# Performance work log

Measured on AMD Instinct MI355X. Metric: run time of the kernel, lower is better.

## Reference

```python
import jax, jax.numpy as jnp
import numpy as np

N, D, K, NUM_PAIRS = 8192, 128, 128, 262144


def setup_inputs() -> dict:
    rng = np.random.default_rng(0)
    labels = rng.integers(0, K, size=N).astype(np.int32)
    # positive pairs: off-diagonal (i,j) with labels[i]==labels[j], same as
    # (diag_mask * match).nonzero() in torch; take a fixed deterministic prefix.
    match = labels[:, None] == labels[None, :]
    np.fill_diagonal(match, False)
    pi, pj = np.nonzero(match)
    assert pi.shape[0] >= NUM_PAIRS
    pos_idx = np.stack([pi[:NUM_PAIRS], pj[:NUM_PAIRS]], axis=1).astype(np.int32)
    # negative pairs: vectorized rejection sampling of (i,j) with labels differing
    neg_chunks, need = [], NUM_PAIRS
    while need > 0:
        cand = rng.integers(0, N, size=(2 * need, 2))
        ok = labels[cand[:, 0]] != labels[cand[:, 1]]
        cand = cand[ok][:need]
        neg_chunks.append(cand)
        need -= cand.shape[0]
    neg_idx = np.concatenate(neg_chunks, axis=0).astype(np.int32)
    key = jax.random.key(0)
    k1, k2 = jax.random.split(key)
    return {
        "Xemb": jax.random.normal(k1, (N, D), dtype=jnp.float32),
        "scores": jax.random.normal(k2, (N,), dtype=jnp.float32),  # unused by forward, kept for signature fidelity
        "h_bias": jnp.asarray(1.0, dtype=jnp.float32),
        "labels": jnp.asarray(labels),
        "pos_idx": jnp.asarray(pos_idx),
        "neg_idx": jnp.asarray(neg_idx),
    }


def reference(Xemb, scores, h_bias, labels, pos_idx, neg_idx):
    bias = jax.nn.softplus(h_bias)
    # positive pairs: squared euclidean distance
    dpos = Xemb[pos_idx[:, 0]] - Xemb[pos_idx[:, 1]]          # [P, D]
    pos_distances_sq = jnp.sum(dpos * dpos, axis=1)           # [P]
    # negative pairs: euclidean distance with margin (softplus bias)
    dneg = Xemb[neg_idx[:, 0]] - Xemb[neg_idx[:, 1]]          # [P, D]
    neg_distances = jnp.sqrt(jnp.sum(dneg * dneg, axis=1))    # [P]
    pos_loss = 0.5 * jnp.mean(pos_distances_sq)
    neg_loss = 0.5 * jnp.mean(jax.nn.relu(bias - neg_distances) ** 2)
    return jnp.stack([pos_loss, neg_loss])  # (cont_pos, cont_neg)
```

## Files before the change

kernel.cpp:

```cpp
#include <hip/hip_runtime.h>
#include <math.h>

#define NPAIRS 262144
#define D_DIM  128
#define TPB    256

__global__ __launch_bounds__(TPB) void pair_kernel(
    const float* __restrict__ X,
    const int*  __restrict__ pos_idx,
    const int*  __restrict__ neg_idx,
    const float* __restrict__ h_bias,
    float* __restrict__ partials)
{
    const int lane  = threadIdx.x & 31;
    const int group = threadIdx.x >> 5;
    const int gid     = (blockIdx.x * TPB + threadIdx.x) >> 5;
    const int ngroups = (gridDim.x * TPB) >> 5;

    const float hb   = h_bias[0];
    const float bias = fmaxf(hb, 0.0f) + log1pf(expf(-fabsf(hb)));

    const float4* __restrict__ X4 = (const float4*)X;
    const int2*  __restrict__ pos2 = (const int2*)pos_idx;
    const int2*  __restrict__ neg2 = (const int2*)neg_idx;

    float posAcc = 0.0f, negAcc = 0.0f;

    for (int p = gid; p < 2 * NPAIRS; p += ngroups) {
        const bool isPos = (p < NPAIRS);
        const int2 ij = isPos ? pos2[p] : neg2[p - NPAIRS];

        const float4 a = X4[ij.x * (D_DIM / 4) + lane];
        const float4 b = X4[ij.y * (D_DIM / 4) + lane];
        const float dx = a.x - b.x, dy = a.y - b.y;
        const float dz = a.z - b.z, dw = a.w - b.w;
        float s = dx * dx + dy * dy + dz * dz + dw * dw;

        s += __shfl_xor(s, 16, 32);
        s += __shfl_xor(s,  8, 32);
        s += __shfl_xor(s,  4, 32);
        s += __shfl_xor(s,  2, 32);
        s += __shfl_xor(s,  1, 32);

        if (isPos) {
            posAcc += s;
        } else {
            float t = bias - sqrtf(s);
            t = fmaxf(t, 0.0f);
            negAcc += t * t;
        }
    }

    __shared__ float sp[TPB / 32], sn[TPB / 32];
    if (lane == 0) { sp[group] = posAcc; sn[group] = negAcc; }
    __syncthreads();
    if (threadIdx.x == 0) {
        float p0 = 0.0f, n0 = 0.0f;
        #pragma unroll
        for (int g = 0; g < TPB / 32; ++g) { p0 += sp[g]; n0 += sn[g]; }
        partials[2 * blockIdx.x]     = p0;
        partials[2 * blockIdx.x + 1] = n0;
    }
}

__global__ __launch_bounds__(TPB) void finalize_kernel(
    const float* __restrict__ partials, int nblk, float* __restrict__ out)
{
    __shared__ float sp[TPB], sn[TPB];
    float p = 0.0f, n = 0.0f;
    for (int b = threadIdx.x; b < nblk; b += TPB) {
        p += partials[2 * b];
        n += partials[2 * b + 1];
    }
    sp[threadIdx.x] = p; sn[threadIdx.x] = n;
    __syncthreads();
    for (int s = TPB / 2; s > 0; s >>= 1) {
        if ((int)threadIdx.x < s) {
            sp[threadIdx.x] += sp[threadIdx.x + s];
            sn[threadIdx.x] += sn[threadIdx.x + s];
        }
        __syncthreads();
    }
    if (threadIdx.x == 0) {
        out[0] = 0.5f * sp[0] / (float)NPAIRS;
        out[1] = 0.5f * sn[0] / (float)NPAIRS;
    }
}

extern "C" void kernel_launch(void* const* d_in, const int* in_sizes, int n_in,
                              void* d_out, int out_size, void* d_ws, size_t ws_size,
                              hipStream_t stream) {
    const float* X       = (const float*)d_in[0];
    const float* h_bias  = (const float*)d_in[2];
    const int*   pos_idx = (const int*)d_in[4];
    const int*   neg_idx = (const int*)d_in[5];
    float*       out      = (float*)d_out;
    float*       partials = (float*)d_ws;

    int nblk = 2048;
    const size_t need = (size_t)nblk * 2 * sizeof(float);
    if (ws_size < need) {
        nblk = (int)(ws_size / (2 * sizeof(float)));
        if (nblk < 1) nblk = 1;
    }

    pair_kernel<<<nblk, TPB, 0, stream>>>(X, pos_idx, neg_idx, h_bias, partials);
    finalize_kernel<<<1, TPB, 0, stream>>>(partials, nblk, out);
}
```

Baseline: 99.05 us.

## Split pos/neg loops, unroll 4 pairs per group, defer reductions, fuse finalize via atomics

Splits the combined loop into separate positive and negative loops, each handling four pairs per 32-lane group per iteration so more gather loads are in flight. Positive pairs accumulate per lane and are reduced with shuffles only once at the end. The second finalize kernel is replaced by per-block atomicAdd into an output that is zeroed with a memset. This trades a kernel launch for atomics and a memset, and makes the float summation order nondeterministic.

```diff
diff --git a/kernel.cpp b/kernel.cpp
--- a/kernel.cpp
+++ b/kernel.cpp
@@ -2,88 +2,110 @@
 #include <math.h>
 
 #define NPAIRS 262144
-#define D_DIM  128
+#define D4     32
 #define TPB    256
+#define NBLK   2048
 
 __global__ __launch_bounds__(TPB) void pair_kernel(
     const float* __restrict__ X,
-    const int*  __restrict__ pos_idx,
-    const int*  __restrict__ neg_idx,
+    const int2*  __restrict__ pos2,
+    const int2*  __restrict__ neg2,
     const float* __restrict__ h_bias,
-    float* __restrict__ partials)
+    float* __restrict__ out)
 {
-    const int lane  = threadIdx.x & 31;
-    const int group = threadIdx.x >> 5;
+    const int lane    = threadIdx.x & 31;
+    const int group   = threadIdx.x >> 5;
     const int gid     = (blockIdx.x * TPB + threadIdx.x) >> 5;
     const int ngroups = (gridDim.x * TPB) >> 5;
+
+    const float4* __restrict__ X4 = (const float4*)X;
 
     const float hb   = h_bias[0];
     const float bias = fmaxf(hb, 0.0f) + log1pf(expf(-fabsf(hb)));
 
-    const float4* __restrict__ X4 = (const float4*)X;
-    const int2*  __restrict__ pos2 = (const int2*)pos_idx;
-    const int2*  __restrict__ neg2 = (const int2*)neg_idx;
+    float posAcc = 0.0f;
+    for (int p = gid; p < NPAIRS; p += 4 * ngroups) {
+        const int2 ij0 = pos2[p];
+        const int2 ij1 = pos2[p +     ngroups];
+        const int2 ij2 = pos2[p + 2 * ngroups];
+        const int2 ij3 = pos2[p + 3 * ngroups];
+        const float4 a0 = X4[ij0.x * D4 + lane], b0 = X4[ij0.y * D4 + lane];
+        const float4 a1 = X4[ij1.x * D4 + lane], b1 = X4[ij1.y * D4 + lane];
+        const float4 a2 = X4[ij2.x * D4 + lane], b2 = X4[ij2.y * D4 + lane];
+        const float4 a3 = X4[ij3.x * D4 + lane], b3 = X4[ij3.y * D4 + lane];
+        float d;
+        d = a0.x - b0.x; posAcc = fmaf(d, d, posAcc);
+        d = a0.y - b0.y; posAcc = fmaf(d, d, posAcc);
+        d = a0.z - b0.z; posAcc = fmaf(d, d, posAcc);
+        d = a0.w - b0.w; posAcc = fmaf(d, d, posAcc);
+        d = a1.x - b1.x; posAcc = fmaf(d, d, posAcc);
+        d = a1.y - b1.y; posAcc = fmaf(d, d, posAcc);
+        d = a1.z - b1.z; posAcc = fmaf(d, d, posAcc);
+        d = a1.w - b1.w; posAcc = fmaf(d, d, posAcc);
+        d = a2.x - b2.x; posAcc = fmaf(d, d, posAcc);
+        d = a2.y - b2.y; posAcc = fmaf(d, d, posAcc);
+        d = a2.z - b2.z; posAcc = fmaf(d, d, posAcc);
+        d = a2.w - b2.w; posAcc = fmaf(d, d, posAcc);
+        d = a3.x - b3.x; posAcc = fmaf(d, d, posAcc);
+        d = a3.y - b3.y; posAcc = fmaf(d, d, posAcc);
+        d = a3.z - b3.z; posAcc = fmaf(d, d, posAcc);
+        d = a3.w - b3.w; posAcc = fmaf(d, d, posAcc);
+    }
 
-    float posAcc = 0.0f, negAcc = 0.0f;
+    float negAcc = 0.0f;
+    for (int p = gid; p < NPAIRS; p += 4 * ngroups) {
+        const int2 ij0 = neg2[p];
+        const int2 ij1 = neg2[p +     ngroups];
+        const int2 ij2 = neg2[p + 2 * ngroups];
+        const int2 ij3 = neg2[p + 3 * ngroups];
+        const float4 a0 = X4[ij0.x * D4 + lane], b0 = X4[ij0.y * D4 + lane];
+        const float4 a1 = X4[ij1.x * D4 + lane], b1 = X4[ij1.y * D4 + lane];
+        const float4 a2 = X4[ij2.x * D4 + lane], b2 = X4[ij2.y * D4 + lane];
+        const float4 a3 = X4[ij3.x * D4 + lane], b3 = X4[ij3.y * D4 + lane];
+        float d;
+        float s0 = 0.f, s1 = 0.f, s2 = 0.f, s3 = 0.f;
+        d = a0.x - b0.x; s0 = fmaf(d, d, s0);
+        d = a0.y - b0.y; s0 = fmaf(d, d, s0);
+        d = a0.z - b0.z; s0 = fmaf(d, d, s0);
+        d = a0.w - b0.w; s0 = fmaf(d, d, s0);
+        d = a1.x - b1.x; s1 = fmaf(d, d, s1);
+        d = a1.y - b1.y; s1 = fmaf(d, d, s1);
+        d = a1.z - b1.z; s1 = fmaf(d, d, s1);
+        d = a1.w - b1.w; s1 = fmaf(d, d, s1);
+        d = a2.x - b2.x; s2 = fmaf(d, d, s2);
+        d = a2.y - b2.y; s2 = fmaf(d, d, s2);
+        d = a2.z - b2.z; s2 = fmaf(d, d, s2);
+        d = a2.w - b2.w; s2 = fmaf(d, d, s2);
+        d = a3.x - b3.x; s3 = fmaf(d, d, s3);
+        d = a3.y - b3.y; s3 = fmaf(d, d, s3);
+        d = a3.z - b3.z; s3 = fmaf(d, d, s3);
+        d = a3.w - b3.w; s3 = fmaf(d, d, s3);
+        #pragma unroll
+        for (int m = 16; m > 0; m >>= 1) {
+            s0 += __shfl_xor(s0, m, 32);
+            s1 += __shfl_xor(s1, m, 32);
+            s2 += __shfl_xor(s2, m, 32);
+            s3 += __shfl_xor(s3, m, 32);
+        }
+        float t;
+        t = fmaxf(bias - sqrtf(s0), 0.f); negAcc = fmaf(t, t, negAcc);
+        t = fmaxf(bias - sqrtf(s1), 0.f); negAcc = fmaf(t, t, negAcc);
+        t = fmaxf(bias - sqrtf(s2), 0.f); negAcc = fmaf(t, t, negAcc);
+        t = fmaxf(bias - sqrtf(s3), 0.f); negAcc = fmaf(t, t, negAcc);
+    }
 
-    for (int p = gid; p < 2 * NPAIRS; p += ngroups) {
-        const bool isPos = (p < NPAIRS);
-        const int2 ij = isPos ? pos2[p] : neg2[p - NPAIRS];
-
-        const float4 a = X4[ij.x * (D_DIM / 4) + lane];
-        const float4 b = X4[ij.y * (D_DIM / 4) + lane];
-        const float dx = a.x - b.x, dy = a.y - b.y;
-        const float dz = a.z - b.z, dw = a.w - b.w;
-        float s = dx * dx + dy * dy + dz * dz + dw * dw;
-
-        s += __shfl_xor(s, 16, 32);
-        s += __shfl_xor(s,  8, 32);
-        s += __shfl_xor(s,  4, 32);
-        s += __shfl_xor(s,  2, 32);
-        s += __shfl_xor(s,  1, 32);
-
-        if (isPos) {
-            posAcc += s;
-        } else {
-            float t = bias - sqrtf(s);
-            t = fmaxf(t, 0.0f);
-            negAcc += t * t;
-        }
-    }
+    #pragma unroll
+    for (int m = 16; m > 0; m >>= 1) posAcc += __shfl_xor(posAcc, m, 32);
 
     __shared__ float sp[TPB / 32], sn[TPB / 32];
     if (lane == 0) { sp[group] = posAcc; sn[group] = negAcc; }
     __syncthreads();
     if (threadIdx.x == 0) {
-        float p0 = 0.0f, n0 = 0.0f;
+        float P = 0.f, Nn = 0.f;
         #pragma unroll
-        for (int g = 0; g < TPB / 32; ++g) { p0 += sp[g]; n0 += sn[g]; }
-        partials[2 * blockIdx.x]     = p0;
-        partials[2 * blockIdx.x + 1] = n0;
-    }
-}
-
-__global__ __launch_bounds__(TPB) void finalize_kernel(
-    const float* __restrict__ partials, int nblk, float* __restrict__ out)
-{
-    __shared__ float sp[TPB], sn[TPB];
-    float p = 0.0f, n = 0.0f;
-    for (int b = threadIdx.x; b < nblk; b += TPB) {
-        p += partials[2 * b];
-        n += partials[2 * b + 1];
-    }
-    sp[threadIdx.x] = p; sn[threadIdx.x] = n;
-    __syncthreads();
-    for (int s = TPB / 2; s > 0; s >>= 1) {
-        if ((int)threadIdx.x < s) {
-            sp[threadIdx.x] += sp[threadIdx.x + s];
-            sn[threadIdx.x] += sn[threadIdx.x + s];
-        }
-        __syncthreads();
-    }
-    if (threadIdx.x == 0) {
-        out[0] = 0.5f * sp[0] / (float)NPAIRS;
-        out[1] = 0.5f * sn[0] / (float)NPAIRS;
+        for (int g = 0; g < TPB / 32; ++g) { P += sp[g]; Nn += sn[g]; }
+        atomicAdd(&out[0], P  * (0.5f / NPAIRS));
+        atomicAdd(&out[1], Nn * (0.5f / NPAIRS));
     }
 }
 
@@ -92,18 +114,10 @@
                               hipStream_t stream) {
     const float* X       = (const float*)d_in[0];
     const float* h_bias  = (const float*)d_in[2];
-    const int*   pos_idx = (const int*)d_in[4];
-    const int*   neg_idx = (const int*)d_in[5];
-    float*       out      = (float*)d_out;
-    float*       partials = (float*)d_ws;
+    const int2*  pos2    = (const int2*)d_in[4];
+    const int2*  neg2    = (const int2*)d_in[5];
+    float*       out     = (float*)d_out;
 
-    int nblk = 2048;
-    const size_t need = (size_t)nblk * 2 * sizeof(float);
-    if (ws_size < need) {
-        nblk = (int)(ws_size / (2 * sizeof(float)));
-        if (nblk < 1) nblk = 1;
-    }
-
-    pair_kernel<<<nblk, TPB, 0, stream>>>(X, pos_idx, neg_idx, h_bias, partials);
-    finalize_kernel<<<1, TPB, 0, stream>>>(partials, nblk, out);
+    hipMemsetAsync(out, 0, (size_t)out_size * sizeof(float), stream);
+    pair_kernel<<<NBLK, TPB, 0, stream>>>(X, pos2, neg2, h_bias, out);
 }
```

Measured after the change: 132.2 us. 33.5% more time.
